# Performance work log

Hardware: AMD Instinct MI355X
Metric: run time of the kernel (lower is better)

Reference implementation:

```python
import jax, jax.numpy as jnp
import numpy as np
import math

D_MODEL = 512
N_HEAD = 8
TAU = 0.5


def _leaky_integrate(x):
    # dx/dt = -x / tau; x + dx/dt  (with tau=0.5 this equals -x)
    return x + (-x / TAU)


def setup_inputs() -> dict:
    key = jax.random.key(0)
    ks = jax.random.split(key, 12)
    B, S, D = 4, 2048, D_MODEL
    s = 1.0 / math.sqrt(D)
    inp = {
        "query": jax.random.normal(ks[0], (B, S, D), jnp.float32),
        "key": jax.random.normal(ks[1], (B, S, D), jnp.float32),
        "value": jax.random.normal(ks[2], (B, S, D), jnp.float32),
        "Wq": jax.random.normal(ks[3], (D, D), jnp.float32) * s,
        "bq": jnp.zeros((D,), jnp.float32),
        "Wk": jax.random.normal(ks[4], (D, D), jnp.float32) * s,
        "bk": jnp.zeros((D,), jnp.float32),
        "Wv": jax.random.normal(ks[5], (D, D), jnp.float32) * s,
        "bv": jnp.zeros((D,), jnp.float32),
        "Wo": jax.random.normal(ks[6], (D, D), jnp.float32) * s,
        "bo": jnp.zeros((D,), jnp.float32),
    }
    return inp


def reference(query, key, value, Wq, bq, Wk, bk, Wv, bv, Wo, bo):
    B, S, D = query.shape
    H = N_HEAD
    dh = D // H
    # linear projections (torch Linear: x @ W^T + b)
    q = query @ Wq.T + bq
    k = key @ Wk.T + bk
    v = value @ Wv.T + bv
    # (B, S, D) -> (B, H, S, dh)
    q = q.reshape(B, S, H, dh).transpose(0, 2, 1, 3)
    k = k.reshape(B, S, H, dh).transpose(0, 2, 1, 3)
    v = v.reshape(B, S, H, dh).transpose(0, 2, 1, 3)
    # leaky integration on q, k
    q = _leaky_integrate(q)
    k = _leaky_integrate(k)
    # scores scaled by sqrt(d_model) (NOT head dim) per the source
    scores = jnp.einsum("bhsd,bhtd->bhst", q, k) / math.sqrt(D_MODEL)
    attn = jax.nn.softmax(scores, axis=-1)
    # conductance-based synapse: elementwise sigmoid AFTER softmax
    attn = jax.nn.sigmoid(attn)
    out = jnp.einsum("bhst,bhtd->bhsd", attn, v)
    out = out.transpose(0, 2, 1, 3).reshape(B, S, D)
    return out @ Wo.T + bo
```

## Files before the change

kernel.cpp:

```cpp
#include <hip/hip_runtime.h>
#include <stdint.h>
#include <math.h>

using u16    = unsigned short;
using short8 = __attribute__((ext_vector_type(8))) short;
using f32x4  = __attribute__((ext_vector_type(4))) float;
using f32x16 = __attribute__((ext_vector_type(16))) float;
using u32x4  = __attribute__((ext_vector_type(4))) uint32_t;

#define DEVI __device__ __forceinline__
#define FENCE asm volatile("" ::: "memory")
#define GPTR(p) ((const __attribute__((address_space(1))) uint32_t*)(p))
#define LPTR(p) ((__attribute__((address_space(3))) uint32_t*)(p))

static constexpr int S  = 2048;
static constexpr int D  = 512;
static constexpr int DH = 64;
static constexpr float C2 = 0.063763906f;

DEVI u16 f2bf(float f){
  uint32_t u = __float_as_uint(f);
  u = u + 0x7FFFu + ((u >> 16) & 1u);
  return (u16)(u >> 16);
}

DEVI uint32_t cvt_pk_bf16(float a, float b){
  uint32_t d;
  asm("v_cvt_pk_bf16_f32 %0, %1, %2" : "=v"(d) : "v"(a), "v"(b));
  return d;
}

__global__ void k_cvtw(const float* __restrict__ a, const float* __restrict__ b,
                       const float* __restrict__ c, const float* __restrict__ d,
                       u16* __restrict__ out){
  int i = blockIdx.x * blockDim.x + threadIdx.x;
  int sel = i >> 16;
  const float* src = sel == 0 ? a : sel == 1 ? b : sel == 2 ? c : d;
  float4 v = reinterpret_cast<const float4*>(src)[i & ((1<<16)-1)];
  uint2 o;
  o.x = (uint32_t)f2bf(v.x) | ((uint32_t)f2bf(v.y) << 16);
  o.y = (uint32_t)f2bf(v.z) | ((uint32_t)f2bf(v.w) << 16);
  reinterpret_cast<uint2*>(out)[i] = o;
}

__global__ __launch_bounds__(512)
void k_gemm_qkv(const float* __restrict__ Xq, const float* __restrict__ Xk,
                const float* __restrict__ Xv, const u16* __restrict__ Wall,
                const float* __restrict__ bq, const float* __restrict__ bk,
                const float* __restrict__ bv,
                u16* __restrict__ Qp, u16* __restrict__ Kp, u16* __restrict__ Vtp)
{
  __shared__ __align__(16) u16 As[2][128*64];
  __shared__ __align__(16) u16 Bs[2][128*64];
  const int tid = threadIdx.x;
  const int w = tid >> 6, l = tid & 63;
  const int wm = w & 3, wn = w >> 2;
  const int m0 = blockIdx.x * 128, n0 = blockIdx.y * 128;
  const int z = blockIdx.z;
  const int srow = l >> 3, sslot = l & 7;

  const float* X = z == 0 ? Xq : (z == 1 ? Xk : Xv);
  const u16*   W = Wall + (size_t)z * 512 * 512;
  const float* bias = z == 0 ? bq : (z == 1 ? bk : bv);
  const float oscale = z == 0 ? C2 : 1.0f;

  const int arow = tid >> 2;
  const int ac   = (tid & 3) * 16;

  f32x4 acc[2][4];
  #pragma unroll
  for (int i = 0; i < 2; i++)
    #pragma unroll
    for (int j = 0; j < 4; j++)
      #pragma unroll
      for (int r = 0; r < 4; r++) acc[i][j][r] = 0.f;

  float4 av[4];
  auto LOADA = [&](int kt){
    #pragma unroll
    for (int j = 0; j < 4; j++)
      av[j] = *reinterpret_cast<const float4*>(&X[(long)(m0 + arow)*D + kt + ac + j*4]);
  };
  auto WRITEA = [&](int buf){
    #pragma unroll
    for (int j2 = 0; j2 < 2; j2++){
      u32x4 p;
      p[0] = cvt_pk_bf16(av[2*j2].x,   av[2*j2].y);
      p[1] = cvt_pk_bf16(av[2*j2].z,   av[2*j2].w);
      p[2] = cvt_pk_bf16(av[2*j2+1].x, av[2*j2+1].y);
      p[3] = cvt_pk_bf16(av[2*j2+1].z, av[2*j2+1].w);
      int slot = ((ac >> 3) + j2) ^ (arow & 7);
      *reinterpret_cast<u32x4*>(&As[buf][arow*64 + slot*8]) = p;
    }
  };
  auto STAGEB = [&](int buf, int kt){
    #pragma unroll
    for (int i = 0; i < 2; i++){
      int r = w*16 + i*8 + srow;
      int scol = (sslot ^ (r & 7)) * 8;
      __builtin_amdgcn_global_load_lds(GPTR(W + (long)(n0 + r)*D + kt + scol),
                                       LPTR(&Bs[buf][(w*16 + i*8)*64]), 16, 0, 0);
    }
  };

  LOADA(0); STAGEB(0, 0);
  asm volatile("s_waitcnt vmcnt(0)" ::: "memory");
  WRITEA(0);
  __syncthreads();

  for (int t = 0; t < 8; t++){
    int buf = t & 1;
    if (t < 7){ STAGEB(buf ^ 1, (t+1)*64); LOADA((t+1)*64); }
    #pragma unroll
    for (int ks = 0; ks < 2; ks++){
      short8 af[2];
      #pragma unroll
      for (int mf = 0; mf < 2; mf++){
        int row = wm*32 + mf*16 + (l & 15);
        int cw = (ks*4 + (l >> 4)) ^ (row & 7);
        af[mf] = *reinterpret_cast<const short8*>(&As[buf][(row*8 + cw)*8]);
      }
      #pragma unroll
      for (int nf = 0; nf < 4; nf++){
        int row = wn*64 + nf*16 + (l & 15);
        int cw = (ks*4 + (l >> 4)) ^ (row & 7);
        short8 bf = *reinterpret_cast<const short8*>(&Bs[buf][(row*8 + cw)*8]);
        #pragma unroll
        for (int mf = 0; mf < 2; mf++)
          acc[mf][nf] = __builtin_amdgcn_mfma_f32_16x16x32_bf16(af[mf], bf, acc[mf][nf], 0, 0, 0);
      }
    }
    asm volatile("s_waitcnt vmcnt(0)" ::: "memory");
    if (t < 7) WRITEA(buf ^ 1);
    __syncthreads();
  }

  #pragma unroll
  for (int mf = 0; mf < 2; mf++){
    #pragma unroll
    for (int nf = 0; nf < 4; nf++){
      int n = n0 + wn*64 + nf*16 + (l & 15);
      float bi = bias[n];
      int h_ = n >> 6, d_ = n & 63;
      if (z == 2){
        int mb = m0 + wm*32 + mf*16 + (l >> 4)*4;
        int b_ = mb >> 11, s_ = mb & 2047;
        uint2 o;
        o.x = (uint32_t)f2bf(acc[mf][nf][0] + bi) | ((uint32_t)f2bf(acc[mf][nf][1] + bi) << 16);
        o.y = (uint32_t)f2bf(acc[mf][nf][2] + bi) | ((uint32_t)f2bf(acc[mf][nf][3] + bi) << 16);
        *reinterpret_cast<uint2*>(&Vtp[((long)((b_*8 + h_)*64 + d_))*2048 + s_]) = o;
      } else {
        u16* outp = z == 0 ? Qp : Kp;
        #pragma unroll
        for (int r = 0; r < 4; r++){
          int m = m0 + wm*32 + mf*16 + (l >> 4)*4 + r;
          int b_ = m >> 11, s_ = m & 2047;
          outp[((long)((b_*8 + h_)*2048 + s_))*64 + d_] = f2bf((acc[mf][nf][r] + bi)*oscale);
        }
      }
    }
  }
}

__global__ __launch_bounds__(512)
void k_gemm_ao(const u16* __restrict__ A, const u16* __restrict__ W,
               const float* __restrict__ bias2, float* __restrict__ outp)
{
  __shared__ __align__(16) u16 As[2][128*64];
  __shared__ __align__(16) u16 Bs[2][128*64];
  const int tid = threadIdx.x;
  const int w = tid >> 6, l = tid & 63;
  const int wm = w & 3, wn = w >> 2;
  const int m0 = blockIdx.x * 128, n0 = blockIdx.y * 128;
  const int srow = l >> 3, sslot = l & 7;

  f32x4 acc[2][4];
  #pragma unroll
  for (int i = 0; i < 2; i++)
    #pragma unroll
    for (int j = 0; j < 4; j++)
      #pragma unroll
      for (int r = 0; r < 4; r++) acc[i][j][r] = 0.f;

  auto STAGE = [&](int buf, int kt){
    #pragma unroll
    for (int i = 0; i < 2; i++){
      int r = w*16 + i*8 + srow;
      int scol = (sslot ^ (r & 7)) * 8;
      int m = m0 + r, k = kt + scol;
      long ga = ((long)(((m >> 11)*8 + (k >> 6))*2048 + (m & 2047)))*64 + (k & 63);
      __builtin_amdgcn_global_load_lds(GPTR(A + ga), LPTR(&As[buf][(w*16 + i*8)*64]), 16, 0, 0);
      long gb = (long)(n0 + r)*D + kt + scol;
      __builtin_amdgcn_global_load_lds(GPTR(W + gb), LPTR(&Bs[buf][(w*16 + i*8)*64]), 16, 0, 0);
    }
  };

  STAGE(0, 0);
  asm volatile("s_waitcnt vmcnt(0)" ::: "memory");
  __builtin_amdgcn_s_barrier();
  FENCE;

  for (int kt = 0; kt < D; kt += 64){
    int buf = (kt >> 6) & 1;
    if (kt + 64 < D) STAGE(buf ^ 1, kt + 64);
    #pragma unroll
    for (int ks = 0; ks < 2; ks++){
      short8 af[2];
      #pragma unroll
      for (int mf = 0; mf < 2; mf++){
        int row = wm*32 + mf*16 + (l & 15);
        int cw = (ks*4 + (l >> 4)) ^ (row & 7);
        af[mf] = *reinterpret_cast<const short8*>(&As[buf][(row*8 + cw)*8]);
      }
      #pragma unroll
      for (int nf = 0; nf < 4; nf++){
        int row = wn*64 + nf*16 + (l & 15);
        int cw = (ks*4 + (l >> 4)) ^ (row & 7);
        short8 bf = *reinterpret_cast<const short8*>(&Bs[buf][(row*8 + cw)*8]);
        #pragma unroll
        for (int mf = 0; mf < 2; mf++)
          acc[mf][nf] = __builtin_amdgcn_mfma_f32_16x16x32_bf16(af[mf], bf, acc[mf][nf], 0, 0, 0);
      }
    }
    asm volatile("s_waitcnt vmcnt(0)" ::: "memory");
    __builtin_amdgcn_s_barrier();
    FENCE;
  }

  #pragma unroll
  for (int mf = 0; mf < 2; mf++)
    #pragma unroll
    for (int nf = 0; nf < 4; nf++){
      int n = n0 + wn*64 + nf*16 + (l & 15);
      float bi = bias2[(m0 >> 11)*512 + n];
      #pragma unroll
      for (int r = 0; r < 4; r++){
        int m = m0 + wm*32 + mf*16 + (l >> 4)*4 + r;
        outp[(long)m*D + n] = acc[mf][nf][r] + bi;
      }
    }
}

__global__ __launch_bounds__(256)
void k_sumv(const u16* __restrict__ Vt, float* __restrict__ SV){
  const int w = threadIdx.x >> 6, l = threadIdx.x & 63;
  const int row = blockIdx.x*4 + w;
  const u16* src = Vt + (long)row * S;
  float s = 0.f;
  #pragma unroll
  for (int j = 0; j < 4; j++){
    short8 v = *reinterpret_cast<const short8*>(&src[j*512 + l*8]);
    #pragma unroll
    for (int e = 0; e < 8; e++)
      s += __uint_as_float(((uint32_t)(u16)v[e]) << 16);
  }
  #pragma unroll
  for (int m = 1; m < 64; m <<= 1) s += __shfl_xor(s, m, 64);
  if (l == 0) SV[row] = s;
}

__global__ __launch_bounds__(256)
void k_bias2(const float* __restrict__ SV, const float* __restrict__ Wo,
             const float* __restrict__ bo, float* __restrict__ bias2){
  const int w = threadIdx.x >> 6, l = threadIdx.x & 63;
  const int idx = blockIdx.x*4 + w;
  const int b = idx >> 9, n = idx & 511;
  float dot = 0.f;
  #pragma unroll
  for (int j = 0; j < 2; j++){
    float4 wv = *reinterpret_cast<const float4*>(&Wo[(long)n*512 + l*8 + j*4]);
    float4 sv = *reinterpret_cast<const float4*>(&SV[b*512 + l*8 + j*4]);
    dot += wv.x*sv.x + wv.y*sv.y + wv.z*sv.z + wv.w*sv.w;
  }
  #pragma unroll
  for (int m = 1; m < 64; m <<= 1) dot += __shfl_xor(dot, m, 64);
  if (l == 0) bias2[idx] = bo[n] + 0.5f * dot;
}

__global__ __launch_bounds__(512, 4)
void k_flash(const u16* __restrict__ Qp, const u16* __restrict__ Kp,
             const u16* __restrict__ Vt, u16* __restrict__ AO)
{
  __shared__ __align__(16) u16 Ks[2][2][64*64];
  __shared__ __align__(16) u16 Vs[2][2][64*64];
  const int tid = threadIdx.x, w = tid >> 6, l = tid & 63;
  const int g = w >> 2, w4 = w & 3;
  const int bh = blockIdx.x & 31, qt = blockIdx.x >> 5;
  const u16* Qb = Qp + (long)bh * S * DH;
  const int hi = l >> 5, ln = l & 31;
  const int srow = l >> 3, sslot = l & 7;

  short8 qfr[4];
  #pragma unroll
  for (int c = 0; c < 4; c++){
    int row = qt*128 + w4*32 + ln;
    qfr[c] = *reinterpret_cast<const short8*>(&Qb[(long)row*DH + c*16 + hi*8]);
  }

  int koff[4], voff[8];
  #pragma unroll
  for (int c = 0; c < 4; c++)
    koff[c] = ln*64 + (((2*c + hi) ^ (ln & 7))*8);
  #pragma unroll
  for (int kf = 0; kf < 2; kf++)
    #pragma unroll
    for (int ch = 0; ch < 2; ch++)
      #pragma unroll
      for (int nf = 0; nf < 2; nf++)
        voff[kf*4 + ch*2 + nf] = (nf*32 + ln)*64 + ((((4*kf + 2*ch) + hi) ^ (ln & 7))*8);

  const u16* kptr = Kp + (long)bh*S*DH + g*4096;
  const u16* vptr = Vt + (long)bh*DH*S + g*64;
  long ksrc[2], vsrc[2];
  #pragma unroll
  for (int i = 0; i < 2; i++){
    int r = w4*16 + i*8 + srow;
    int sc = (sslot ^ (r & 7))*8;
    ksrc[i] = (long)r*64 + sc;
    vsrc[i] = (long)r*S + sc;
  }

  auto STAGE = [&](int buf){
    #pragma unroll
    for (int i = 0; i < 2; i++){
      __builtin_amdgcn_global_load_lds(GPTR(kptr + ksrc[i]), LPTR(&Ks[g][buf][(w4*16 + i*8)*64]), 16, 0, 0);
      __builtin_amdgcn_global_load_lds(GPTR(vptr + vsrc[i]), LPTR(&Vs[g][buf][(w4*16 + i*8)*64]), 16, 0, 0);
    }
    kptr += 8192;
    vptr += 128;
  };

  f32x16 zero16;
  #pragma unroll
  for (int r = 0; r < 16; r++) zero16[r] = 0.f;
  f32x16 oacc[2];
  #pragma unroll
  for (int j = 0; j < 2; j++)
    #pragma unroll
    for (int r = 0; r < 16; r++) oacc[j][r] = 0.f;
  float lsum = 0.f;

  STAGE(0);
  asm volatile("s_waitcnt vmcnt(0)" ::: "memory");
  __builtin_amdgcn_s_barrier();
  FENCE;

  const u16* KB = &Ks[g][0][0];
  const u16* VB = &Vs[g][0][0];

  for (int tp = 0; tp < 8; tp++){
    #pragma unroll
    for (int tt = 0; tt < 2; tt++){
      int t = tp*2 + tt;
      if (t < 15) STAGE(tt ^ 1);
      #pragma unroll
      for (int kf = 0; kf < 2; kf++){
        __builtin_amdgcn_s_setprio(1);
        short8 kf0 = *reinterpret_cast<const short8*>(KB + koff[0] + tt*4096 + kf*2048);
        f32x16 sacc = __builtin_amdgcn_mfma_f32_32x32x16_bf16(kf0, qfr[0], zero16, 0, 0, 0);
        #pragma unroll
        for (int c = 1; c < 4; c++){
          short8 kfrag = *reinterpret_cast<const short8*>(KB + koff[c] + tt*4096 + kf*2048);
          sacc = __builtin_amdgcn_mfma_f32_32x32x16_bf16(kfrag, qfr[c], sacc, 0, 0, 0);
        }
        __builtin_amdgcn_s_setprio(0);
        uint32_t pk[8];
        #pragma unroll
        for (int j = 0; j < 8; j++){
          float e0 = __builtin_amdgcn_exp2f(sacc[2*j]);
          float e1 = __builtin_amdgcn_exp2f(sacc[2*j+1]);
          lsum += e0 + e1;
          pk[j] = cvt_pk_bf16(e0, e1);
        }
        #pragma unroll
        for (int ch = 0; ch < 2; ch++){
          auto s1 = __builtin_amdgcn_permlane32_swap(pk[ch*4+0], pk[ch*4+2], false, false);
          auto s2 = __builtin_amdgcn_permlane32_swap(pk[ch*4+1], pk[ch*4+3], false, false);
          u32x4 av = { (uint32_t)s1[0], (uint32_t)s2[0], (uint32_t)s1[1], (uint32_t)s2[1] };
          short8 af = __builtin_bit_cast(short8, av);
          __builtin_amdgcn_s_setprio(1);
          #pragma unroll
          for (int nf = 0; nf < 2; nf++){
            short8 vfrag = *reinterpret_cast<const short8*>(VB + voff[kf*4 + ch*2 + nf] + tt*4096);
            oacc[nf] = __builtin_amdgcn_mfma_f32_32x32x16_bf16(af, vfrag, oacc[nf], 0, 0, 0);
          }
          __builtin_amdgcn_s_setprio(0);
        }
      }
      asm volatile("s_waitcnt vmcnt(0)" ::: "memory");
      __builtin_amdgcn_s_barrier();
      FENCE;
    }
  }

  lsum += __shfl_xor(lsum, 32, 64);
  float* OB = (float*)Ks;
  float* LB = (float*)Vs;
  if (g == 1){
    #pragma unroll
    for (int r = 0; r < 16; r++){
      int qrow = (r & 3) + 8*(r >> 2) + 4*hi;
      #pragma unroll
      for (int nf = 0; nf < 2; nf++)
        OB[w4*2048 + qrow*64 + nf*32 + ln] = oacc[nf][r];
    }
    if (hi == 0) LB[w4*32 + ln] = lsum;
  }
  __syncthreads();
  if (g == 0){
    float l2 = LB[w4*32 + ln];
    float linv = 0.25f / (lsum + l2);
    #pragma unroll
    for (int r = 0; r < 16; r++){
      int qrow = (r & 3) + 8*(r >> 2) + 4*hi;
      float sc = __shfl(linv, qrow, 64);
      int s_ = qt*128 + w4*32 + qrow;
      #pragma unroll
      for (int nf = 0; nf < 2; nf++){
        float o = oacc[nf][r] + OB[w4*2048 + qrow*64 + nf*32 + ln];
        AO[((long)bh*S + s_)*DH + nf*32 + ln] = f2bf(o * sc);
      }
    }
  }
}

extern "C" void kernel_launch(void* const* d_in, const int* in_sizes, int n_in,
                              void* d_out, int out_size, void* d_ws, size_t ws_size,
                              hipStream_t stream)
{
  const float* query = (const float*)d_in[0];
  const float* key_  = (const float*)d_in[1];
  const float* value = (const float*)d_in[2];
  const float* Wq = (const float*)d_in[3];
  const float* bq = (const float*)d_in[4];
  const float* Wk = (const float*)d_in[5];
  const float* bk = (const float*)d_in[6];
  const float* Wv = (const float*)d_in[7];
  const float* bv = (const float*)d_in[8];
  const float* Wo = (const float*)d_in[9];
  const float* bo = (const float*)d_in[10];

  char* ws = (char*)d_ws;
  const size_t XSZ = (size_t)8192 * 512 * 2;
  const size_t WSZ = (size_t)512 * 512 * 2;
  u16* AO  = (u16*)(ws);
  u16* wqb = (u16*)(ws + XSZ);
  u16* wob = (u16*)(ws + XSZ + 3*WSZ);
  u16* Qp  = (u16*)(ws + XSZ + 4*WSZ);
  u16* Kp  = (u16*)(ws + 2*XSZ + 4*WSZ);
  u16* Vtp = (u16*)(ws + 3*XSZ + 4*WSZ);
  float* SV    = (float*)(ws + 4*XSZ + 4*WSZ);
  float* bias2 = (float*)(ws + 4*XSZ + 4*WSZ + 8192);

  k_cvtw<<<(4<<16)/256, 256, 0, stream>>>(Wq, Wk, Wv, Wo, wqb);

  dim3 gq(64, 4, 3);
  k_gemm_qkv<<<gq, 512, 0, stream>>>(query, key_, value, wqb, bq, bk, bv, Qp, Kp, Vtp);

  k_sumv <<<512, 256, 0, stream>>>(Vtp, SV);
  k_bias2<<<512, 256, 0, stream>>>(SV, Wo, bo, bias2);

  k_flash<<<512, 512, 0, stream>>>(Qp, Kp, Vtp, AO);

  dim3 gg(64, 4);
  k_gemm_ao<<<gg, 512, 0, stream>>>(AO, wob, bias2, (float*)d_out);
}
```

Before: 98.22 us.

## Deepen load pipelines in flash and output GEMM kernels with multi-buffered LDS

The flash kernel now stages 32-key tiles into a 4-deep ring of LDS buffers with three tiles in flight. It uses partial vmcnt waits instead of draining all loads each step, and the swizzle patterns are reworked to fit the new tile shapes. The output GEMM switches to a 3-stage triple-buffered prefetch with partial waits, and the QKV GEMM drops its explicit vmcnt drain and reorders its loads. The aim is to hide global-load latency behind MFMA work, in exchange for more LDS use, more barriers per key, and fragile hand-written wait counts.

```diff
diff --git a/kernel.cpp b/kernel.cpp
--- a/kernel.cpp
+++ b/kernel.cpp
@@ -104,13 +104,12 @@
   };
 
   LOADA(0); STAGEB(0, 0);
-  asm volatile("s_waitcnt vmcnt(0)" ::: "memory");
   WRITEA(0);
   __syncthreads();
 
   for (int t = 0; t < 8; t++){
     int buf = t & 1;
-    if (t < 7){ STAGEB(buf ^ 1, (t+1)*64); LOADA((t+1)*64); }
+    if (t < 7){ LOADA((t+1)*64); STAGEB(buf ^ 1, (t+1)*64); }
     #pragma unroll
     for (int ks = 0; ks < 2; ks++){
       short8 af[2];
@@ -130,7 +129,6 @@
           acc[mf][nf] = __builtin_amdgcn_mfma_f32_16x16x32_bf16(af[mf], bf, acc[mf][nf], 0, 0, 0);
       }
     }
-    asm volatile("s_waitcnt vmcnt(0)" ::: "memory");
     if (t < 7) WRITEA(buf ^ 1);
     __syncthreads();
   }
@@ -166,8 +164,8 @@
 void k_gemm_ao(const u16* __restrict__ A, const u16* __restrict__ W,
                const float* __restrict__ bias2, float* __restrict__ outp)
 {
-  __shared__ __align__(16) u16 As[2][128*64];
-  __shared__ __align__(16) u16 Bs[2][128*64];
+  __shared__ __align__(16) u16 As[3][128*64];
+  __shared__ __align__(16) u16 Bs[3][128*64];
   const int tid = threadIdx.x;
   const int w = tid >> 6, l = tid & 63;
   const int wm = w & 3, wn = w >> 2;
@@ -195,14 +193,15 @@
     }
   };
 
-  STAGE(0, 0);
-  asm volatile("s_waitcnt vmcnt(0)" ::: "memory");
+  STAGE(0, 0); STAGE(1, 64);
+  asm volatile("s_waitcnt vmcnt(4)" ::: "memory");
   __builtin_amdgcn_s_barrier();
   FENCE;
 
-  for (int kt = 0; kt < D; kt += 64){
-    int buf = (kt >> 6) & 1;
-    if (kt + 64 < D) STAGE(buf ^ 1, kt + 64);
+  #pragma unroll
+  for (int t = 0; t < 8; t++){
+    const int buf = t % 3;
+    if (t + 2 < 8) STAGE((t + 2) % 3, (t + 2)*64);
     #pragma unroll
     for (int ks = 0; ks < 2; ks++){
       short8 af[2];
@@ -222,9 +221,12 @@
           acc[mf][nf] = __builtin_amdgcn_mfma_f32_16x16x32_bf16(af[mf], bf, acc[mf][nf], 0, 0, 0);
       }
     }
-    asm volatile("s_waitcnt vmcnt(0)" ::: "memory");
-    __builtin_amdgcn_s_barrier();
-    FENCE;
+    if (t < 7){
+      if (t < 6) asm volatile("s_waitcnt vmcnt(4)" ::: "memory");
+      else       asm volatile("s_waitcnt vmcnt(0)" ::: "memory");
+      __builtin_amdgcn_s_barrier();
+      FENCE;
+    }
   }
 
   #pragma unroll
@@ -281,14 +283,13 @@
 void k_flash(const u16* __restrict__ Qp, const u16* __restrict__ Kp,
              const u16* __restrict__ Vt, u16* __restrict__ AO)
 {
-  __shared__ __align__(16) u16 Ks[2][2][64*64];
-  __shared__ __align__(16) u16 Vs[2][2][64*64];
+  __shared__ __align__(16) u16 Ks[2][4][32*64];
+  __shared__ __align__(16) u16 Vs[2][4][64*32];
   const int tid = threadIdx.x, w = tid >> 6, l = tid & 63;
   const int g = w >> 2, w4 = w & 3;
   const int bh = blockIdx.x & 31, qt = blockIdx.x >> 5;
   const u16* Qb = Qp + (long)bh * S * DH;
   const int hi = l >> 5, ln = l & 31;
-  const int srow = l >> 3, sslot = l & 7;
 
   short8 qfr[4];
   #pragma unroll
@@ -297,37 +298,30 @@
     qfr[c] = *reinterpret_cast<const short8*>(&Qb[(long)row*DH + c*16 + hi*8]);
   }
 
-  int koff[4], voff[8];
+  int koff[4], voff[4];
   #pragma unroll
   for (int c = 0; c < 4; c++)
-    koff[c] = ln*64 + (((2*c + hi) ^ (ln & 7))*8);
-  #pragma unroll
-  for (int kf = 0; kf < 2; kf++)
-    #pragma unroll
-    for (int ch = 0; ch < 2; ch++)
-      #pragma unroll
-      for (int nf = 0; nf < 2; nf++)
-        voff[kf*4 + ch*2 + nf] = (nf*32 + ln)*64 + ((((4*kf + 2*ch) + hi) ^ (ln & 7))*8);
-
-  const u16* kptr = Kp + (long)bh*S*DH + g*4096;
-  const u16* vptr = Vt + (long)bh*DH*S + g*64;
-  long ksrc[2], vsrc[2];
-  #pragma unroll
-  for (int i = 0; i < 2; i++){
-    int r = w4*16 + i*8 + srow;
-    int sc = (sslot ^ (r & 7))*8;
-    ksrc[i] = (long)r*64 + sc;
-    vsrc[i] = (long)r*S + sc;
-  }
+    koff[c] = ln*64 + (((2*c + hi) ^ ((ln ^ (ln >> 3)) & 7))*8);
+  #pragma unroll
+  for (int ch = 0; ch < 2; ch++)
+    #pragma unroll
+    for (int nf = 0; nf < 2; nf++){
+      int row = nf*32 + ln;
+      voff[ch*2 + nf] = row*32 + (((2*ch + hi) ^ ((row ^ (row >> 2)) & 3))*8);
+    }
+
+  const u16* kptr = Kp + (long)bh*S*DH + g*2048;
+  const u16* vptr = Vt + (long)bh*DH*S + g*32;
+  const int rK = w4*8 + (l >> 3), sK = l & 7;
+  const int rV = w4*16 + (l >> 2), sV = l & 3;
+  const long ksrc = (long)rK*64 + ((sK ^ ((rK ^ (rK >> 3)) & 7))*8);
+  const long vsrc = (long)rV*S  + ((sV ^ ((rV ^ (rV >> 2)) & 3))*8);
 
   auto STAGE = [&](int buf){
-    #pragma unroll
-    for (int i = 0; i < 2; i++){
-      __builtin_amdgcn_global_load_lds(GPTR(kptr + ksrc[i]), LPTR(&Ks[g][buf][(w4*16 + i*8)*64]), 16, 0, 0);
-      __builtin_amdgcn_global_load_lds(GPTR(vptr + vsrc[i]), LPTR(&Vs[g][buf][(w4*16 + i*8)*64]), 16, 0, 0);
-    }
-    kptr += 8192;
-    vptr += 128;
+    __builtin_amdgcn_global_load_lds(GPTR(kptr + ksrc), LPTR(&Ks[g][buf][w4*512]), 16, 0, 0);
+    __builtin_amdgcn_global_load_lds(GPTR(vptr + vsrc), LPTR(&Vs[g][buf][w4*512]), 16, 0, 0);
+    kptr += 4096;
+    vptr += 64;
   };
 
   f32x16 zero16;
@@ -340,58 +334,73 @@
     for (int r = 0; r < 16; r++) oacc[j][r] = 0.f;
   float lsum = 0.f;
 
-  STAGE(0);
-  asm volatile("s_waitcnt vmcnt(0)" ::: "memory");
+  const u16* KB = &Ks[g][0][0];
+  const u16* VB = &Vs[g][0][0];
+
+  auto COMPUTE = [&](int buf){
+    const u16* KT = KB + buf*2048;
+    const u16* VT = VB + buf*2048;
+    __builtin_amdgcn_s_setprio(1);
+    short8 k0 = *reinterpret_cast<const short8*>(KT + koff[0]);
+    f32x16 sacc = __builtin_amdgcn_mfma_f32_32x32x16_bf16(k0, qfr[0], zero16, 0, 0, 0);
+    #pragma unroll
+    for (int c = 1; c < 4; c++){
+      short8 kfrag = *reinterpret_cast<const short8*>(KT + koff[c]);
+      sacc = __builtin_amdgcn_mfma_f32_32x32x16_bf16(kfrag, qfr[c], sacc, 0, 0, 0);
+    }
+    __builtin_amdgcn_s_setprio(0);
+    uint32_t pk[8];
+    #pragma unroll
+    for (int j = 0; j < 8; j++){
+      float e0 = __builtin_amdgcn_exp2f(sacc[2*j]);
+      float e1 = __builtin_amdgcn_exp2f(sacc[2*j+1]);
+      lsum += e0 + e1;
+      pk[j] = cvt_pk_bf16(e0, e1);
+    }
+    #pragma unroll
+    for (int ch = 0; ch < 2; ch++){
+      auto s1 = __builtin_amdgcn_permlane32_swap(pk[ch*4+0], pk[ch*4+2], false, false);
+      auto s2 = __builtin_amdgcn_permlane32_swap(pk[ch*4+1], pk[ch*4+3], false, false);
+      u32x4 av = { (uint32_t)s1[0], (uint32_t)s2[0], (uint32_t)s1[1], (uint32_t)s2[1] };
+      short8 af = __builtin_bit_cast(short8, av);
+      __builtin_amdgcn_s_setprio(1);
+      #pragma unroll
+      for (int nf = 0; nf < 2; nf++){
+        short8 vfrag = *reinterpret_cast<const short8*>(VT + voff[ch*2 + nf]);
+        oacc[nf] = __builtin_amdgcn_mfma_f32_32x32x16_bf16(af, vfrag, oacc[nf], 0, 0, 0);
+      }
+      __builtin_amdgcn_s_setprio(0);
+    }
+  };
+
+  STAGE(0); STAGE(1); STAGE(2);
+  asm volatile("s_waitcnt vmcnt(4)" ::: "memory");
   __builtin_amdgcn_s_barrier();
   FENCE;
 
-  const u16* KB = &Ks[g][0][0];
-  const u16* VB = &Vs[g][0][0];
-
-  for (int tp = 0; tp < 8; tp++){
-    #pragma unroll
-    for (int tt = 0; tt < 2; tt++){
-      int t = tp*2 + tt;
-      if (t < 15) STAGE(tt ^ 1);
-      #pragma unroll
-      for (int kf = 0; kf < 2; kf++){
-        __builtin_amdgcn_s_setprio(1);
-        short8 kf0 = *reinterpret_cast<const short8*>(KB + koff[0] + tt*4096 + kf*2048);
-        f32x16 sacc = __builtin_amdgcn_mfma_f32_32x32x16_bf16(kf0, qfr[0], zero16, 0, 0, 0);
-        #pragma unroll
-        for (int c = 1; c < 4; c++){
-          short8 kfrag = *reinterpret_cast<const short8*>(KB + koff[c] + tt*4096 + kf*2048);
-          sacc = __builtin_amdgcn_mfma_f32_32x32x16_bf16(kfrag, qfr[c], sacc, 0, 0, 0);
-        }
-        __builtin_amdgcn_s_setprio(0);
-        uint32_t pk[8];
-        #pragma unroll
-        for (int j = 0; j < 8; j++){
-          float e0 = __builtin_amdgcn_exp2f(sacc[2*j]);
-          float e1 = __builtin_amdgcn_exp2f(sacc[2*j+1]);
-          lsum += e0 + e1;
-          pk[j] = cvt_pk_bf16(e0, e1);
-        }
-        #pragma unroll
-        for (int ch = 0; ch < 2; ch++){
-          auto s1 = __builtin_amdgcn_permlane32_swap(pk[ch*4+0], pk[ch*4+2], false, false);
-          auto s2 = __builtin_amdgcn_permlane32_swap(pk[ch*4+1], pk[ch*4+3], false, false);
-          u32x4 av = { (uint32_t)s1[0], (uint32_t)s2[0], (uint32_t)s1[1], (uint32_t)s2[1] };
-          short8 af = __builtin_bit_cast(short8, av);
-          __builtin_amdgcn_s_setprio(1);
-          #pragma unroll
-          for (int nf = 0; nf < 2; nf++){
-            short8 vfrag = *reinterpret_cast<const short8*>(VB + voff[kf*4 + ch*2 + nf] + tt*4096);
-            oacc[nf] = __builtin_amdgcn_mfma_f32_32x32x16_bf16(af, vfrag, oacc[nf], 0, 0, 0);
-          }
-          __builtin_amdgcn_s_setprio(0);
-        }
-      }
-      asm volatile("s_waitcnt vmcnt(0)" ::: "memory");
+  for (int tp = 0; tp < 7; tp++){
+    #pragma unroll
+    for (int tt = 0; tt < 4; tt++){
+      STAGE((tt + 3) & 3);
+      COMPUTE(tt);
+      asm volatile("s_waitcnt vmcnt(4)" ::: "memory");
       __builtin_amdgcn_s_barrier();
       FENCE;
     }
   }
+  STAGE(3);
+  COMPUTE(0);
+  asm volatile("s_waitcnt vmcnt(4)" ::: "memory");
+  __builtin_amdgcn_s_barrier(); FENCE;
+  COMPUTE(1);
+  asm volatile("s_waitcnt vmcnt(2)" ::: "memory");
+  __builtin_amdgcn_s_barrier(); FENCE;
+  COMPUTE(2);
+  asm volatile("s_waitcnt vmcnt(0)" ::: "memory");
+  __builtin_amdgcn_s_barrier(); FENCE;
+  COMPUTE(3);
+
+  __syncthreads();
 
   lsum += __shfl_xor(lsum, 32, 64);
   float* OB = (float*)Ks;
```

Result: faster. 95.55 us (-2.7%).
